# Kernel optimization log

Measured on AMD Instinct MI355X. Metric: run time of the kernel, lower is better.

Reference implementation:

```python
import jax, jax.numpy as jnp
import numpy as np

K = 3
PAD = 1
EPS = 1e-5


def _conv2d(x, w, b):
    y = jax.lax.conv_general_dilated(x, w, window_strides=(1, 1), padding='SAME',
                                     dimension_numbers=('NCHW', 'OIHW', 'NCHW'))
    return y + b[None, :, None, None]


def _bn(x, g, beta, m, v):
    inv = jax.lax.rsqrt(v + EPS)
    return (x - m[None, :, None, None]) * (g * inv)[None, :, None, None] + beta[None, :, None, None]


def _deform_conv2d(x, offset, w, b):
    # torchvision deform_conv2d (v1, no mask), stride=1, pad=1, 3x3 kernel.
    B, Cin, H, W = x.shape
    Cout = w.shape[0]
    # offset: [B, 2*K*K, H, W] -> (dy, dx) per kernel tap
    off = offset.reshape(B, K * K, 2, H, W)
    dy, dx = off[:, :, 0], off[:, :, 1]                     # [B, K2, H, W]
    ii, jj = jnp.meshgrid(jnp.arange(K), jnp.arange(K), indexing='ij')
    ki = (ii.reshape(-1) - PAD).astype(x.dtype)             # [K2]
    kj = (jj.reshape(-1) - PAD).astype(x.dtype)
    py = jnp.arange(H, dtype=x.dtype)[None, None, :, None] + ki[None, :, None, None] + dy
    px = jnp.arange(W, dtype=x.dtype)[None, None, None, :] + kj[None, :, None, None] + dx
    y0 = jnp.floor(py)
    x0 = jnp.floor(px)
    wy = py - y0
    wx = px - x0
    flat = x.reshape(B, Cin, H * W)

    def gather(yc, xc):
        valid = ((yc >= 0) & (yc < H) & (xc >= 0) & (xc < W)).astype(x.dtype)
        yi = jnp.clip(yc, 0, H - 1).astype(jnp.int32)
        xi = jnp.clip(xc, 0, W - 1).astype(jnp.int32)
        idx = (yi * W + xi).reshape(B, -1)                  # [B, K2*H*W]
        g = jax.vmap(lambda f, i: f[:, i])(flat, idx)       # [B, Cin, K2*H*W]
        return g.reshape(B, Cin, K * K, H, W) * valid[:, None]

    v = (gather(y0,     x0    ) * ((1 - wy) * (1 - wx))[:, None]
         + gather(y0,     x0 + 1) * ((1 - wy) * wx)[:, None]
         + gather(y0 + 1, x0    ) * (wy * (1 - wx))[:, None]
         + gather(y0 + 1, x0 + 1) * (wy * wx)[:, None])     # [B, Cin, K2, H, W]
    out = jnp.einsum('bckhw,ock->bohw', v, w.reshape(Cout, Cin, K * K))
    return out + b[None, :, None, None]


def setup_inputs() -> dict:
    key = jax.random.key(0)
    ks = jax.random.split(key, 12)
    d = {}
    d['x'] = jax.random.normal(ks[0], (32, 3, 64, 64), jnp.float32)
    d['offset1_w'] = jax.random.normal(ks[1], (18, 3, 3, 3), jnp.float32) * 0.05
    d['offset1_b'] = jnp.zeros((18,), jnp.float32)
    d['conv1_w'] = jax.random.normal(ks[2], (64, 3, 3, 3), jnp.float32) * 0.1
    d['conv1_b'] = jnp.zeros((64,), jnp.float32)
    d['bn1_gamma'] = jnp.ones((64,), jnp.float32)
    d['bn1_beta'] = jnp.zeros((64,), jnp.float32)
    d['bn1_mean'] = jnp.zeros((64,), jnp.float32)
    d['bn1_var'] = jax.random.uniform(ks[3], (64,), jnp.float32, 0.5, 1.5)
    d['offset2_w'] = jax.random.normal(ks[4], (18, 64, 3, 3), jnp.float32) * 0.02
    d['offset2_b'] = jnp.zeros((18,), jnp.float32)
    d['conv2_w'] = jax.random.normal(ks[5], (128, 64, 3, 3), jnp.float32) * 0.05
    d['conv2_b'] = jnp.zeros((128,), jnp.float32)
    d['bn2_gamma'] = jnp.ones((128,), jnp.float32)
    d['bn2_beta'] = jnp.zeros((128,), jnp.float32)
    d['bn2_mean'] = jnp.zeros((128,), jnp.float32)
    d['bn2_var'] = jax.random.uniform(ks[6], (128,), jnp.float32, 0.5, 1.5)
    d['fc1_w'] = jax.random.normal(ks[7], (256, 128), jnp.float32) * 0.08
    d['fc1_b'] = jnp.zeros((256,), jnp.float32)
    d['fc2_w'] = jax.random.normal(ks[8], (200, 256), jnp.float32) * 0.06
    d['fc2_b'] = jnp.zeros((200,), jnp.float32)
    return d


def reference(x, offset1_w, offset1_b, conv1_w, conv1_b, bn1_gamma, bn1_beta, bn1_mean, bn1_var,
              offset2_w, offset2_b, conv2_w, conv2_b, bn2_gamma, bn2_beta, bn2_mean, bn2_var,
              fc1_w, fc1_b, fc2_w, fc2_b):
    # Eval-mode forward (dropout layers are identity / deterministic).
    off1 = _conv2d(x, offset1_w, offset1_b)
    h = _deform_conv2d(x, off1, conv1_w, conv1_b)
    h = jax.nn.relu(_bn(h, bn1_gamma, bn1_beta, bn1_mean, bn1_var))
    off2 = _conv2d(h, offset2_w, offset2_b)
    h = _deform_conv2d(h, off2, conv2_w, conv2_b)
    h = jax.nn.relu(_bn(h, bn2_gamma, bn2_beta, bn2_mean, bn2_var))
    h = h.mean(axis=(2, 3))                                 # global avg pool -> [B, 128]
    h = jax.nn.relu(h @ fc1_w.T + fc1_b)
    return h @ fc2_w.T + fc2_b
```

## Files before the change

### kernel.cpp

```cpp
#include <hip/hip_runtime.h>

#define EPS 1e-5f

#define W1OT 0
#define W1B  1024
#define W2T  4096
#define W2OB 40960
#define SC1  59392
#define SH1  59456
#define SC2  59520
#define SH2  59648
#define POOL 59776
#define XP   65536
#define H1B  589824
#define W1B_U   2048
#define W2T_U   8192
#define W2OB_U  81920
#define H1B_U   1179648

typedef __attribute__((ext_vector_type(8))) short bhalf8;
typedef __attribute__((ext_vector_type(8))) unsigned short u16x8;
typedef __attribute__((ext_vector_type(4))) float f32x4;
typedef __attribute__((ext_vector_type(4))) uint u32x4;

#define APAD 40

struct Tap { int i00, i01, i10, i11; float w00, w01, w10, w11; };

__device__ __forceinline__ Tap make_tap(float py, float px) {
    float y0f = floorf(py), x0f = floorf(px);
    float wy = py - y0f, wx = px - x0f;
    bool by0 = (y0f >= 0.f)  && (y0f < 64.f);
    bool by1 = (y0f >= -1.f) && (y0f < 63.f);
    bool bx0 = (x0f >= 0.f)  && (x0f < 64.f);
    bool bx1 = (x0f >= -1.f) && (x0f < 63.f);
    int y0 = min(max((int)y0f, 0), 63);
    int y1 = min(max((int)y0f + 1, 0), 63);
    int x0 = min(max((int)x0f, 0), 63);
    int x1 = min(max((int)x0f + 1, 0), 63);
    Tap tp;
    tp.i00 = y0 * 64 + x0; tp.i01 = y0 * 64 + x1;
    tp.i10 = y1 * 64 + x0; tp.i11 = y1 * 64 + x1;
    tp.w00 = (by0 && bx0) ? (1.f - wy) * (1.f - wx) : 0.f;
    tp.w01 = (by0 && bx1) ? (1.f - wy) * wx         : 0.f;
    tp.w10 = (by1 && bx0) ? wy * (1.f - wx)         : 0.f;
    tp.w11 = (by1 && bx1) ? wy * wx                 : 0.f;
    return tp;
}

__device__ __forceinline__ ushort f2bf(float f) {
    union { float f; uint u; } a; a.f = f;
    uint u = a.u;
    return (ushort)((u + 0x7fffu + ((u >> 16) & 1u)) >> 16);
}
__device__ __forceinline__ float bf2f(ushort u) {
    union { uint u; float f; } a; a.u = ((uint)u) << 16;
    return a.f;
}

__device__ __forceinline__ uint cvtpk_bf16(float a, float b) {
    uint r;
    asm("v_cvt_pk_bf16_f32 %0, %1, %2" : "=v"(r) : "v"(a), "v"(b));
    return r;
}

__device__ __forceinline__ f32x4 evenf(uint4 u) {
    union { uint u; float f; } a;
    f32x4 r;
    a.u = u.x << 16; r[0] = a.f;
    a.u = u.y << 16; r[1] = a.f;
    a.u = u.z << 16; r[2] = a.f;
    a.u = u.w << 16; r[3] = a.f;
    return r;
}
__device__ __forceinline__ f32x4 oddf(uint4 u) {
    union { uint u; float f; } a;
    f32x4 r;
    a.u = u.x & 0xffff0000u; r[0] = a.f;
    a.u = u.y & 0xffff0000u; r[1] = a.f;
    a.u = u.z & 0xffff0000u; r[2] = a.f;
    a.u = u.w & 0xffff0000u; r[3] = a.f;
    return r;
}

__device__ __forceinline__ void gl_lds16(const void* g, void* l) {
    __builtin_amdgcn_global_load_lds(
        (const __attribute__((address_space(1))) unsigned int*)g,
        (__attribute__((address_space(3))) unsigned int*)l, 16, 0, 0);
}

__global__ __launch_bounds__(256) void k_prep(
    const float* __restrict__ x,
    const float* __restrict__ o1w, const float* __restrict__ c1w,
    const float* __restrict__ o2w, const float* __restrict__ c2w,
    const float* __restrict__ c1b, const float* __restrict__ g1,
    const float* __restrict__ be1, const float* __restrict__ m1,
    const float* __restrict__ v1,
    const float* __restrict__ c2b, const float* __restrict__ g2,
    const float* __restrict__ be2, const float* __restrict__ m2,
    const float* __restrict__ v2,
    float* __restrict__ ws) {
    int tid = blockIdx.x * 256 + threadIdx.x;
    ushort* wsu = (ushort*)ws;
    if (tid < 648) {
        int co = tid % 18, tc = tid / 18, c = tc & 3, t = tc >> 2;
        ws[W1OT + tid] = (c < 3) ? o1w[(co * 3 + c) * 9 + t] : 0.f;
    } else if (tid < 2696) {
        int i = tid - 648;
        int n = i >> 5, k = i & 31;
        float v = 0.f;
        if (k < 27) { int c = k % 3, t = k / 3; v = c1w[(n * 3 + c) * 9 + t]; }
        wsu[W1B_U + i] = f2bf(v);
    } else if (tid < 76424) {
        int i = tid - 2696;
        int c = i & 63, n = (i >> 6) & 127, t = i >> 13;
        wsu[W2T_U + i] = f2bf(c2w[(n * 64 + c) * 9 + t]);
    } else if (tid < 94856) {
        int i = tid - 76424;
        int j = i & 7, r = (i >> 3) & 15, q = (i >> 7) & 3;
        int nt = (i >> 9) & 1, ks = (i >> 10) & 1, t = i >> 11;
        int n = nt * 16 + r;
        int c = ks * 32 + q * 8 + j;
        float v = (n < 18) ? o2w[(n * 64 + c) * 9 + t] : 0.f;
        wsu[W2OB_U + i] = f2bf(v);
    } else if (tid < 94920) {
        int i = tid - 94856;
        float s = g1[i] * rsqrtf(v1[i] + EPS);
        ws[SC1 + i] = s;
        ws[SH1 + i] = (c1b[i] - m1[i]) * s + be1[i];
    } else if (tid < 95048) {
        int i = tid - 94920;
        float s = g2[i] * rsqrtf(v2[i] + EPS);
        ws[SC2 + i] = s;
        ws[SH2 + i] = (c2b[i] - m2[i]) * s + be2[i];
    } else if (tid < 99144) {
        ws[POOL + tid - 95048] = 0.f;
    } else if (tid < 230216) {
        int i = tid - 99144;
        int b = i >> 12, hw = i & 4095;
        const float* xpp = x + (size_t)b * 3 * 4096 + hw;
        f32x4 o;
        o[0] = xpp[0]; o[1] = xpp[4096]; o[2] = xpp[8192]; o[3] = 0.f;
        *(f32x4*)(ws + XP + (size_t)i * 4) = o;
    }
}

__global__ __launch_bounds__(256, 4) void k_def1(
    const float* __restrict__ o1b, float* __restrict__ ws) {
    __shared__ ushort Alds[256 * APAD];
    __shared__ ushort Blds[64 * APAD];
    __shared__ float wo[648];
    __shared__ float scl[128];
    int tid = threadIdx.x;
    for (int i = tid; i < 648; i += 256) wo[i] = ws[W1OT + i];
    if (tid < 128) scl[tid] = ws[SC1 + tid];
    {
        const ushort* src = (const ushort*)ws + W1B_U;
        if (tid < 128) {
            int n = tid >> 1, half = (tid & 1) * 16;
            *(uint4*)(Blds + n * APAD + half)     = *(const uint4*)(src + n * 32 + half);
            *(uint4*)(Blds + n * APAD + half + 8) = *(const uint4*)(src + n * 32 + half + 8);
        }
    }
    int g = blockIdx.x;
    int b = (g & 7) * 4 + ((g >> 3) & 3);
    int row0 = (g >> 5) * 4;
    int h = row0 + (tid >> 6), w = tid & 63;
    const float* xp = ws + XP + (size_t)b * 16384;

    float off[18];
#pragma unroll
    for (int i = 0; i < 18; ++i) off[i] = o1b[i];
    __syncthreads();
#pragma unroll
    for (int t = 0; t < 9; ++t) {
        int yy = h + t / 3 - 1, xx = w + t % 3 - 1;
        f32x4 pv = (f32x4)0.f;
        if (yy >= 0 && yy < 64 && xx >= 0 && xx < 64)
            pv = *(const f32x4*)(xp + (yy * 64 + xx) * 4);
#pragma unroll
        for (int c = 0; c < 3; ++c) {
            const float* wp = wo + (t * 4 + c) * 18;
#pragma unroll
            for (int co = 0; co < 18; ++co) off[co] += pv[c] * wp[co];
        }
    }
    ushort ob[32];
#pragma unroll
    for (int i = 0; i < 32; ++i) ob[i] = 0;
#pragma unroll
    for (int t = 0; t < 9; ++t) {
        Tap tp = make_tap((float)(h + t / 3 - 1) + off[2 * t],
                          (float)(w + t % 3 - 1) + off[2 * t + 1]);
        f32x4 c00 = *(const f32x4*)(xp + tp.i00 * 4);
        f32x4 c01 = *(const f32x4*)(xp + tp.i01 * 4);
        f32x4 c10 = *(const f32x4*)(xp + tp.i10 * 4);
        f32x4 c11 = *(const f32x4*)(xp + tp.i11 * 4);
        f32x4 vt = tp.w00 * c00 + tp.w01 * c01 + tp.w10 * c10 + tp.w11 * c11;
        ob[t * 3 + 0] = f2bf(vt[0]);
        ob[t * 3 + 1] = f2bf(vt[1]);
        ob[t * 3 + 2] = f2bf(vt[2]);
    }
    {
        ushort* ar = Alds + tid * APAD;
#pragma unroll
        for (int i = 0; i < 4; ++i)
            *(uint4*)(ar + i * 8) = *(const uint4*)(ob + i * 8);
    }
    __syncthreads();

    int lane = tid & 63, wv = tid >> 6;
    int r = lane & 15, q = lane >> 4;
    bhalf8 bf[4];
#pragma unroll
    for (int nt = 0; nt < 4; ++nt)
        bf[nt] = *(const bhalf8*)(Blds + (nt * 16 + r) * APAD + q * 8);
    f32x4 acc[4][4];
#pragma unroll
    for (int mt = 0; mt < 4; ++mt) {
        bhalf8 af = *(const bhalf8*)(Alds + (wv * 64 + mt * 16 + r) * APAD + q * 8);
#pragma unroll
        for (int nt = 0; nt < 4; ++nt)
            acc[mt][nt] = __builtin_amdgcn_mfma_f32_16x16x32_bf16(af, bf[nt], (f32x4)0.f, 0, 0, 0);
    }
    ushort* hb = (ushort*)ws + H1B_U + (size_t)(b * 4096 + row0 * 64) * 64;
#pragma unroll
    for (int nt = 0; nt < 4; ++nt) {
        int col = nt * 16 + r;
        float s0 = scl[col], s1 = scl[64 + col];
#pragma unroll
        for (int mt = 0; mt < 4; ++mt) {
            int pxl = wv * 64 + mt * 16 + q * 4;
#pragma unroll
            for (int rr = 0; rr < 4; ++rr)
                hb[(size_t)(pxl + rr) * 64 + col] =
                    f2bf(fmaxf(acc[mt][nt][rr] * s0 + s1, 0.f));
        }
    }
}

__global__ __launch_bounds__(256, 4) void k_def2(
    const float* __restrict__ o2b, float* __restrict__ ws) {
    __shared__ __align__(16) char smem[37376];
    float* offL = (float*)(smem + 32768);
    int g = blockIdx.x;
    int b = (g & 7) * 4 + ((g >> 3) & 3);
    int row = g >> 5;
    int tid = threadIdx.x, lane = tid & 63, wv = tid >> 6;
    int r = lane & 15, q = lane >> 4;
    int px = wv * 16 + r;
    const ushort* hb = (const ushort*)ws + H1B_U + (size_t)b * 262144;
    const ushort* wB = (const ushort*)ws + W2T_U;
    const ushort* btl = (const ushort*)ws + W2OB_U + lane * 8;
    int sOff[4];
#pragma unroll
    for (int i = 0; i < 4; ++i) {
        int lin = wv * 4096 + i * 1024 + lane * 16;
        sOff[i] = lin ^ (((lin >> 7) & 7) << 4);
    }
#pragma unroll
    for (int i = 0; i < 4; ++i)
        gl_lds16((const char*)wB + sOff[i], smem + wv * 4096 + i * 1024);

    f32x4 acc2[2];
    acc2[0] = (f32x4)0.f; acc2[1] = (f32x4)0.f;
#pragma unroll
    for (int t = 0; t < 9; ++t) {
        int yy = row + t / 3 - 1;
        int xx = px + t % 3 - 1;
        bool val = (yy >= 0 && yy < 64 && xx >= 0 && xx < 64);
        int yyc = min(max(yy, 0), 63), xxc = min(max(xx, 0), 63);
        const ushort* ap = hb + (size_t)(yyc * 64 + xxc) * 64 + q * 8;
#pragma unroll
        for (int ks = 0; ks < 2; ++ks) {
            bhalf8 af = val ? *(const bhalf8*)(ap + ks * 32) : (bhalf8)(short)0;
#pragma unroll
            for (int nt = 0; nt < 2; ++nt) {
                bhalf8 bf = *(const bhalf8*)(btl + (size_t)((t * 2 + ks) * 2 + nt) * 512);
                acc2[nt] = __builtin_amdgcn_mfma_f32_16x16x32_bf16(af, bf, acc2[nt], 0, 0, 0);
            }
        }
    }
#pragma unroll
    for (int nt = 0; nt < 2; ++nt) {
        int n = nt * 16 + r;
        if (n < 18) {
            float bias = o2b[n];
#pragma unroll
            for (int rr = 0; rr < 4; ++rr)
                offL[(wv * 16 + q * 4 + rr) * 18 + n] = acc2[nt][rr] + bias;
        }
    }
    __syncthreads();

    f32x4 acc[8];
#pragma unroll
    for (int j = 0; j < 8; ++j) acc[j] = (f32x4)0.f;

    Tap tp[2];
    uint4 gq[2][8];
    {
        float oy = offL[px * 18 + 0];
        float ox = offL[px * 18 + 1];
        tp[0] = make_tap((float)(row - 1) + oy, (float)(px - 1) + ox);
        int o00 = tp[0].i00 * 64 + q * 8;
        int o01 = tp[0].i01 * 64 + q * 8;
        int o10 = tp[0].i10 * 64 + q * 8;
        int o11 = tp[0].i11 * 64 + q * 8;
        gq[0][0] = *(const uint4*)(hb + o00);
        gq[0][1] = *(const uint4*)(hb + o01);
        gq[0][2] = *(const uint4*)(hb + o10);
        gq[0][3] = *(const uint4*)(hb + o11);
        gq[0][4] = *(const uint4*)(hb + o00 + 32);
        gq[0][5] = *(const uint4*)(hb + o01 + 32);
        gq[0][6] = *(const uint4*)(hb + o10 + 32);
        gq[0][7] = *(const uint4*)(hb + o11 + 32);
    }

#pragma unroll
    for (int t = 0; t < 9; ++t) {
        const int cur = t & 1, nxt = (t + 1) & 1;
        if (t < 8) {
            float oy = offL[px * 18 + 2 * (t + 1)];
            float ox = offL[px * 18 + 2 * (t + 1) + 1];
            tp[nxt] = make_tap((float)(row + (t + 1) / 3 - 1) + oy,
                               (float)(px + (t + 1) % 3 - 1) + ox);
            int o00 = tp[nxt].i00 * 64 + q * 8;
            int o01 = tp[nxt].i01 * 64 + q * 8;
            int o10 = tp[nxt].i10 * 64 + q * 8;
            int o11 = tp[nxt].i11 * 64 + q * 8;
            gq[nxt][0] = *(const uint4*)(hb + o00);
            gq[nxt][1] = *(const uint4*)(hb + o01);
            gq[nxt][2] = *(const uint4*)(hb + o10);
            gq[nxt][3] = *(const uint4*)(hb + o11);
            gq[nxt][4] = *(const uint4*)(hb + o00 + 32);
            gq[nxt][5] = *(const uint4*)(hb + o01 + 32);
            gq[nxt][6] = *(const uint4*)(hb + o10 + 32);
            gq[nxt][7] = *(const uint4*)(hb + o11 + 32);
        }
        float w00 = tp[cur].w00, w01 = tp[cur].w01;
        float w10 = tp[cur].w10, w11 = tp[cur].w11;
        bhalf8 af0, af1;
        {
            f32x4 ve = w00 * evenf(gq[cur][0]) + w01 * evenf(gq[cur][1])
                     + w10 * evenf(gq[cur][2]) + w11 * evenf(gq[cur][3]);
            f32x4 vo = w00 * oddf(gq[cur][0]) + w01 * oddf(gq[cur][1])
                     + w10 * oddf(gq[cur][2]) + w11 * oddf(gq[cur][3]);
            u32x4 uu;
            uu[0] = cvtpk_bf16(ve[0], vo[0]);
            uu[1] = cvtpk_bf16(ve[1], vo[1]);
            uu[2] = cvtpk_bf16(ve[2], vo[2]);
            uu[3] = cvtpk_bf16(ve[3], vo[3]);
            af0 = __builtin_bit_cast(bhalf8, uu);
        }
        {
            f32x4 ve = w00 * evenf(gq[cur][4]) + w01 * evenf(gq[cur][5])
                     + w10 * evenf(gq[cur][6]) + w11 * evenf(gq[cur][7]);
            f32x4 vo = w00 * oddf(gq[cur][4]) + w01 * oddf(gq[cur][5])
                     + w10 * oddf(gq[cur][6]) + w11 * oddf(gq[cur][7]);
            u32x4 uu;
            uu[0] = cvtpk_bf16(ve[0], vo[0]);
            uu[1] = cvtpk_bf16(ve[1], vo[1]);
            uu[2] = cvtpk_bf16(ve[2], vo[2]);
            uu[3] = cvtpk_bf16(ve[3], vo[3]);
            af1 = __builtin_bit_cast(bhalf8, uu);
        }
        __builtin_amdgcn_sched_barrier(0);
        if (t < 8) asm volatile("s_waitcnt vmcnt(8)" ::: "memory");
        else       asm volatile("s_waitcnt vmcnt(0)" ::: "memory");
        __builtin_amdgcn_s_barrier();
        __builtin_amdgcn_sched_barrier(0);
        if (t < 8) {
            const char* wsrc = (const char*)wB + (t + 1) * 16384;
            char* dst = smem + nxt * 16384 + wv * 4096;
#pragma unroll
            for (int i = 0; i < 4; ++i)
                gl_lds16(wsrc + sOff[i], dst + i * 1024);
        }
        const ushort* Bq = (const ushort*)(smem + cur * 16384);
#pragma unroll
        for (int nt = 0; nt < 8; ++nt) {
            int us = ((nt * 16 + r) * 64 + q * 8) ^ ((r & 7) << 3);
            bhalf8 bf = *(const bhalf8*)(Bq + us);
            acc[nt] = __builtin_amdgcn_mfma_f32_16x16x32_bf16(af0, bf, acc[nt], 0, 0, 0);
        }
#pragma unroll
        for (int nt = 0; nt < 8; ++nt) {
            int us = ((nt * 16 + r) * 64 + 32 + q * 8) ^ ((r & 7) << 3);
            bhalf8 bf = *(const bhalf8*)(Bq + us);
            acc[nt] = __builtin_amdgcn_mfma_f32_16x16x32_bf16(af1, bf, acc[nt], 0, 0, 0);
        }
    }
    const float* sc = ws + SC2;
    const float* sh = ws + SH2;
    float* pool = ws + POOL;
#pragma unroll
    for (int nt = 0; nt < 8; ++nt) {
        int col = nt * 16 + r;
        float s0 = sc[col], s1 = sh[col];
        float s = 0.f;
#pragma unroll
        for (int rr = 0; rr < 4; ++rr)
            s += fmaxf(acc[nt][rr] * s0 + s1, 0.f);
        s += __shfl_xor(s, 16);
        s += __shfl_xor(s, 32);
        if (lane < 16) atomicAdd(&pool[b * 128 + col], s);
    }
}

__global__ __launch_bounds__(256) void k_fc(
    const float* __restrict__ w1, const float* __restrict__ b1,
    const float* __restrict__ w2, const float* __restrict__ b2,
    const float* __restrict__ ws, float* __restrict__ out) {
    int b = blockIdx.x, o = threadIdx.x;
    __shared__ float pl[128];
    __shared__ float hl[256];
    if (o < 128) pl[o] = ws[POOL + b * 128 + o] * (1.f / 4096.f);
    __syncthreads();
    float s = b1[o];
    const float* wp = w1 + o * 128;
#pragma unroll 8
    for (int c = 0; c < 128; ++c) s += pl[c] * wp[c];
    hl[o] = fmaxf(s, 0.f);
    __syncthreads();
    if (o < 200) {
        float s2 = b2[o];
        const float* wp2 = w2 + o * 256;
#pragma unroll 8
        for (int c = 0; c < 256; ++c) s2 += hl[c] * wp2[c];
        out[b * 200 + o] = s2;
    }
}

extern "C" void kernel_launch(void* const* d_in, const int* in_sizes, int n_in,
                              void* d_out, int out_size, void* d_ws, size_t ws_size,
                              hipStream_t stream) {
    const float* x   = (const float*)d_in[0];
    const float* o1w = (const float*)d_in[1];
    const float* o1b = (const float*)d_in[2];
    const float* c1w = (const float*)d_in[3];
    const float* c1b = (const float*)d_in[4];
    const float* g1  = (const float*)d_in[5];
    const float* be1 = (const float*)d_in[6];
    const float* m1  = (const float*)d_in[7];
    const float* v1  = (const float*)d_in[8];
    const float* o2w = (const float*)d_in[9];
    const float* o2b = (const float*)d_in[10];
    const float* c2w = (const float*)d_in[11];
    const float* c2b = (const float*)d_in[12];
    const float* g2  = (const float*)d_in[13];
    const float* be2 = (const float*)d_in[14];
    const float* m2  = (const float*)d_in[15];
    const float* v2  = (const float*)d_in[16];
    const float* f1w = (const float*)d_in[17];
    const float* f1b = (const float*)d_in[18];
    const float* f2w = (const float*)d_in[19];
    const float* f2b = (const float*)d_in[20];
    float* ws  = (float*)d_ws;
    float* out = (float*)d_out;

    k_prep<<<900, 256, 0, stream>>>(x, o1w, c1w, o2w, c2w,
                                    c1b, g1, be1, m1, v1,
                                    c2b, g2, be2, m2, v2, ws);
    k_def1<<<512, 256, 0, stream>>>(o1b, ws);
    k_def2<<<2048, 256, 0, stream>>>(o2b, ws);
    k_fc<<<32, 256, 0, stream>>>(f1w, f1b, f2w, f2b, ws, out);
}
```

Before: 286.1 us.

## Load conv2 weights directly from global in MFMA fragment layout, drop LDS staging

```diff
diff --git a/kernel.cpp b/kernel.cpp
--- a/kernel.cpp
+++ b/kernel.cpp
@@ -19,7 +19,6 @@
 #define H1B_U   1179648
 
 typedef __attribute__((ext_vector_type(8))) short bhalf8;
-typedef __attribute__((ext_vector_type(8))) unsigned short u16x8;
 typedef __attribute__((ext_vector_type(4))) float f32x4;
 typedef __attribute__((ext_vector_type(4))) uint u32x4;
 
@@ -53,10 +52,6 @@
     uint u = a.u;
     return (ushort)((u + 0x7fffu + ((u >> 16) & 1u)) >> 16);
 }
-__device__ __forceinline__ float bf2f(ushort u) {
-    union { uint u; float f; } a; a.u = ((uint)u) << 16;
-    return a.f;
-}
 
 __device__ __forceinline__ uint cvtpk_bf16(float a, float b) {
     uint r;
@@ -81,12 +76,6 @@
     a.u = u.z & 0xffff0000u; r[2] = a.f;
     a.u = u.w & 0xffff0000u; r[3] = a.f;
     return r;
-}
-
-__device__ __forceinline__ void gl_lds16(const void* g, void* l) {
-    __builtin_amdgcn_global_load_lds(
-        (const __attribute__((address_space(1))) unsigned int*)g,
-        (__attribute__((address_space(3))) unsigned int*)l, 16, 0, 0);
 }
 
 __global__ __launch_bounds__(256) void k_prep(
@@ -113,7 +102,10 @@
         wsu[W1B_U + i] = f2bf(v);
     } else if (tid < 76424) {
         int i = tid - 2696;
-        int c = i & 63, n = (i >> 6) & 127, t = i >> 13;
+        int j = i & 7, lane = (i >> 3) & 63, sub = i >> 9;
+        int nt = sub & 7, ks = (sub >> 3) & 1, t = sub >> 4;
+        int r = lane & 15, q = lane >> 4;
+        int n = nt * 16 + r, c = ks * 32 + q * 8 + j;
         wsu[W2T_U + i] = f2bf(c2w[(n * 64 + c) * 9 + t]);
     } else if (tid < 94856) {
         int i = tid - 76424;
@@ -241,8 +233,7 @@
 
 __global__ __launch_bounds__(256, 4) void k_def2(
     const float* __restrict__ o2b, float* __restrict__ ws) {
-    __shared__ __align__(16) char smem[37376];
-    float* offL = (float*)(smem + 32768);
+    __shared__ float offL[64 * 18];
     int g = blockIdx.x;
     int b = (g & 7) * 4 + ((g >> 3) & 3);
     int row = g >> 5;
@@ -250,17 +241,8 @@
     int r = lane & 15, q = lane >> 4;
     int px = wv * 16 + r;
     const ushort* hb = (const ushort*)ws + H1B_U + (size_t)b * 262144;
-    const ushort* wB = (const ushort*)ws + W2T_U;
     const ushort* btl = (const ushort*)ws + W2OB_U + lane * 8;
-    int sOff[4];
-#pragma unroll
-    for (int i = 0; i < 4; ++i) {
-        int lin = wv * 4096 + i * 1024 + lane * 16;
-        sOff[i] = lin ^ (((lin >> 7) & 7) << 4);
-    }
-#pragma unroll
-    for (int i = 0; i < 4; ++i)
-        gl_lds16((const char*)wB + sOff[i], smem + wv * 4096 + i * 1024);
+    const ushort* wtl = (const ushort*)ws + W2T_U + lane * 8;
 
     f32x4 acc2[2];
     acc2[0] = (f32x4)0.f; acc2[1] = (f32x4)0.f;
@@ -292,6 +274,10 @@
         }
     }
     __syncthreads();
+    float2 o2v[9];
+#pragma unroll
+    for (int t = 0; t < 9; ++t)
+        o2v[t] = *(const float2*)(offL + px * 18 + 2 * t);
 
     f32x4 acc[8];
 #pragma unroll
@@ -300,9 +286,7 @@
     Tap tp[2];
     uint4 gq[2][8];
     {
-        float oy = offL[px * 18 + 0];
-        float ox = offL[px * 18 + 1];
-        tp[0] = make_tap((float)(row - 1) + oy, (float)(px - 1) + ox);
+        tp[0] = make_tap((float)(row - 1) + o2v[0].x, (float)(px - 1) + o2v[0].y);
         int o00 = tp[0].i00 * 64 + q * 8;
         int o01 = tp[0].i01 * 64 + q * 8;
         int o10 = tp[0].i10 * 64 + q * 8;
@@ -321,10 +305,8 @@
     for (int t = 0; t < 9; ++t) {
         const int cur = t & 1, nxt = (t + 1) & 1;
         if (t < 8) {
-            float oy = offL[px * 18 + 2 * (t + 1)];
-            float ox = offL[px * 18 + 2 * (t + 1) + 1];
-            tp[nxt] = make_tap((float)(row + (t + 1) / 3 - 1) + oy,
-                               (float)(px + (t + 1) % 3 - 1) + ox);
+            tp[nxt] = make_tap((float)(row + (t + 1) / 3 - 1) + o2v[t + 1].x,
+                               (float)(px + (t + 1) % 3 - 1) + o2v[t + 1].y);
             int o00 = tp[nxt].i00 * 64 + q * 8;
             int o01 = tp[nxt].i01 * 64 + q * 8;
             int o10 = tp[nxt].i10 * 64 + q * 8;
@@ -365,29 +347,14 @@
             uu[3] = cvtpk_bf16(ve[3], vo[3]);
             af1 = __builtin_bit_cast(bhalf8, uu);
         }
-        __builtin_amdgcn_sched_barrier(0);
-        if (t < 8) asm volatile("s_waitcnt vmcnt(8)" ::: "memory");
-        else       asm volatile("s_waitcnt vmcnt(0)" ::: "memory");
-        __builtin_amdgcn_s_barrier();
-        __builtin_amdgcn_sched_barrier(0);
-        if (t < 8) {
-            const char* wsrc = (const char*)wB + (t + 1) * 16384;
-            char* dst = smem + nxt * 16384 + wv * 4096;
-#pragma unroll
-            for (int i = 0; i < 4; ++i)
-                gl_lds16(wsrc + sOff[i], dst + i * 1024);
-        }
-        const ushort* Bq = (const ushort*)(smem + cur * 16384);
 #pragma unroll
         for (int nt = 0; nt < 8; ++nt) {
-            int us = ((nt * 16 + r) * 64 + q * 8) ^ ((r & 7) << 3);
-            bhalf8 bf = *(const bhalf8*)(Bq + us);
+            bhalf8 bf = *(const bhalf8*)(wtl + (size_t)((t * 2 + 0) * 8 + nt) * 512);
             acc[nt] = __builtin_amdgcn_mfma_f32_16x16x32_bf16(af0, bf, acc[nt], 0, 0, 0);
         }
 #pragma unroll
         for (int nt = 0; nt < 8; ++nt) {
-            int us = ((nt * 16 + r) * 64 + 32 + q * 8) ^ ((r & 7) << 3);
-            bhalf8 bf = *(const bhalf8*)(Bq + us);
+            bhalf8 bf = *(const bhalf8*)(wtl + (size_t)((t * 2 + 1) * 8 + nt) * 512);
             acc[nt] = __builtin_amdgcn_mfma_f32_16x16x32_bf16(af1, bf, acc[nt], 0, 0, 0);
         }
     }
```

Result: slower. 325.3 us (+13.7%).
